# Kernel optimization log

Hardware: AMD Instinct MI355X
Metric: run time of the kernel (lower is better)

Reference implementation:

```python
import jax, jax.numpy as jnp
import numpy as np

OUT = 50000   # out_features = connectivity rows
IN = 50000    # in_features  = connectivity cols
NNZ = 1_600_000  # avg degree 32
B = 512       # batch (leading dims of x)


def setup_inputs() -> dict:
    key = jax.random.key(0)
    k1, k2, k3, k4 = jax.random.split(key, 4)
    x = jax.random.normal(k1, (B, IN), dtype=jnp.float32)
    rows = jax.random.randint(k2, (NNZ,), 0, OUT, dtype=jnp.int32)
    cols = jax.random.randint(k3, (NNZ,), 0, IN, dtype=jnp.int32)
    indices = jnp.stack([rows, cols])            # [2, NNZ] COO indices
    values = jax.random.normal(k4, (NNZ,), dtype=jnp.float32)
    bias = jnp.zeros((OUT, 1), dtype=jnp.float32)  # module initializes bias to zeros
    return {"x": x, "indices": indices, "values": values, "bias": bias}


def reference(x, indices, values, bias):
    # feature_dim=-1: permute features to dim 0 -> x_t is (IN, B)
    row, col = indices[0], indices[1]
    x_t = x.T                                    # (IN, B)
    # spmm: for each nnz, values[e] * x_t[col[e]] accumulated into row[e]
    contrib = values[:, None] * x_t[col]         # (NNZ, B)
    y = jax.ops.segment_sum(contrib, row, num_segments=OUT)  # (OUT, B)
    y = y + bias                                 # bias is (OUT, 1), broadcasts
    return y.T                                   # permute back -> (B, OUT)
```

## Files before the change

### kernel.cpp

```cpp
#include <hip/hip_runtime.h>
#include <hip/hip_bf16.h>


typedef float f32x4 __attribute__((ext_vector_type(4)));

#define CAP 96

__global__ void zero_i32_kernel(int* __restrict__ p, int n) {
    int i = blockIdx.x * blockDim.x + threadIdx.x;
    if (i < n) p[i] = 0;
}

__global__ __launch_bounds__(256) void build_kernel(
        const float* __restrict__ x, __hip_bfloat16* __restrict__ xT,
        int rows_x, int cols_x, int tbx, int tbtot,
        const int* __restrict__ erows, const int* __restrict__ ecols,
        const float* __restrict__ evals, int nnz,
        int* __restrict__ cursor, int2* __restrict__ edges) {
    __shared__ __hip_bfloat16 T[64][72];
    const int bid = blockIdx.x;

    if (bid < tbtot) {
        const int bx = bid % tbx;
        const int by = bid / tbx;
        const int c0 = bx * 64;
        const int r0 = by * 64;
        const int t  = threadIdx.x;

        {
            const int tx = t & 15, ty = t >> 4;
            const int c = c0 + tx * 4;
            for (int p = 0; p < 4; ++p) {
                const int rl = ty + p * 16;
                const int r = r0 + rl;
                float fx = 0.f, fy = 0.f, fz = 0.f, fw = 0.f;
                if (r < rows_x && c + 3 < cols_x) {
                    f32x4 f = __builtin_nontemporal_load(
                        (const f32x4*)(x + (size_t)r * cols_x + c));
                    fx = f.x; fy = f.y; fz = f.z; fw = f.w;
                } else if (r < rows_x) {
                    const float* p0 = x + (size_t)r * cols_x;
                    if (c + 0 < cols_x) fx = p0[c + 0];
                    if (c + 1 < cols_x) fy = p0[c + 1];
                    if (c + 2 < cols_x) fz = p0[c + 2];
                    if (c + 3 < cols_x) fw = p0[c + 3];
                }
                T[tx * 4 + 0][rl] = __float2bfloat16(fx);
                T[tx * 4 + 1][rl] = __float2bfloat16(fy);
                T[tx * 4 + 2][rl] = __float2bfloat16(fz);
                T[tx * 4 + 3][rl] = __float2bfloat16(fw);
            }
        }
        __syncthreads();
        {
            const int cl0 = t >> 3;
            const int rq  = t & 7;
            const int rl  = rq * 8;
            const int r   = r0 + rl;
            for (int q = 0; q < 2; ++q) {
                const int cl = q * 32 + cl0;
                const int c  = c0 + cl;
                if (c < cols_x) {
                    if (r + 7 < rows_x) {
                        *(uint4*)(xT + (size_t)c * rows_x + r) =
                            *(const uint4*)&T[cl][rl];
                    } else {
                        for (int j = 0; j < 8 && r + j < rows_x; ++j)
                            xT[(size_t)c * rows_x + r + j] = T[cl][rl + j];
                    }
                }
            }
        }
    } else {
        const int e = (bid - tbtot) * 256 + threadIdx.x;
        if (e < nnz) {
            const int   r = __builtin_nontemporal_load(erows + e);
            const int   c = __builtin_nontemporal_load(ecols + e);
            const float v = __builtin_nontemporal_load(evals + e);
            const int   p = atomicAdd(&cursor[r], 1);
            if (p < CAP)
                edges[(size_t)r * CAP + p] = make_int2(c, __float_as_int(v));
        }
    }
}

__device__ __forceinline__ float bf_lo(unsigned u) {
    return __uint_as_float(u << 16);
}
__device__ __forceinline__ float bf_hi(unsigned u) {
    return __uint_as_float(u & 0xffff0000u);
}

__device__ __forceinline__ void row_accum(
        const ushort* __restrict__ xb, const int2* __restrict__ edges,
        int e0, int e1, int B,
        float& a0, float& a1, float& a2, float& a3,
        float& a4, float& a5, float& a6, float& a7) {
    int e = e0;
    for (; e + 2 <= e1; e += 2) {
        const int2 d0 = edges[e];
        const int2 d1 = edges[e + 1];
        const uint4 u0 = *(const uint4*)(xb + (size_t)d0.x * B);
        const uint4 u1 = *(const uint4*)(xb + (size_t)d1.x * B);
        const float v0 = __int_as_float(d0.y);
        const float v1 = __int_as_float(d1.y);
        a0 += v0 * bf_lo(u0.x); a1 += v0 * bf_hi(u0.x);
        a2 += v0 * bf_lo(u0.y); a3 += v0 * bf_hi(u0.y);
        a4 += v0 * bf_lo(u0.z); a5 += v0 * bf_hi(u0.z);
        a6 += v0 * bf_lo(u0.w); a7 += v0 * bf_hi(u0.w);
        a0 += v1 * bf_lo(u1.x); a1 += v1 * bf_hi(u1.x);
        a2 += v1 * bf_lo(u1.y); a3 += v1 * bf_hi(u1.y);
        a4 += v1 * bf_lo(u1.z); a5 += v1 * bf_hi(u1.z);
        a6 += v1 * bf_lo(u1.w); a7 += v1 * bf_hi(u1.w);
    }
    if (e < e1) {
        const int2 d0 = edges[e];
        const uint4 u0 = *(const uint4*)(xb + (size_t)d0.x * B);
        const float v0 = __int_as_float(d0.y);
        a0 += v0 * bf_lo(u0.x); a1 += v0 * bf_hi(u0.x);
        a2 += v0 * bf_lo(u0.y); a3 += v0 * bf_hi(u0.y);
        a4 += v0 * bf_lo(u0.z); a5 += v0 * bf_hi(u0.z);
        a6 += v0 * bf_lo(u0.w); a7 += v0 * bf_hi(u0.w);
    }
}

__global__ __launch_bounds__(1024) void spmm_fused_kernel(
        const ushort* __restrict__ xT,
        const int* __restrict__ cursor,
        const int2* __restrict__ edges,
        const float* __restrict__ bias,
        float* __restrict__ outp,
        int OUTn) {
    __shared__ float Ty[16][516];
    const int w    = threadIdx.x >> 6;
    const int lane = threadIdx.x & 63;
    const int r    = blockIdx.x * 16 + w;
    const int B    = 512;

    float a0 = 0.f, a1 = 0.f, a2 = 0.f, a3 = 0.f;
    float a4 = 0.f, a5 = 0.f, a6 = 0.f, a7 = 0.f;
    {
        const int deg = min(cursor[r], CAP);
        const int e0  = r * CAP;
        const float bv = bias[r];
        const ushort* xb = xT + (size_t)(lane << 3);
        row_accum(xb, edges, e0, e0 + deg, B, a0, a1, a2, a3, a4, a5, a6, a7);
        a0 += bv; a1 += bv; a2 += bv; a3 += bv;
        a4 += bv; a5 += bv; a6 += bv; a7 += bv;
    }

    {
        float* p = &Ty[w][lane << 3];
        f32x4 f0, f1;
        f0.x = a0; f0.y = a1; f0.z = a2; f0.w = a3;
        f1.x = a4; f1.y = a5; f1.z = a6; f1.w = a7;
        *(f32x4*)(p)     = f0;
        *(f32x4*)(p + 4) = f1;
    }
    __syncthreads();
    {
        const int b  = threadIdx.x & 511;
        const int rq = (threadIdx.x >> 9) << 3;
        f32x4 f0, f1;
        f0.x = Ty[rq + 0][b]; f0.y = Ty[rq + 1][b];
        f0.z = Ty[rq + 2][b]; f0.w = Ty[rq + 3][b];
        f1.x = Ty[rq + 4][b]; f1.y = Ty[rq + 5][b];
        f1.z = Ty[rq + 6][b]; f1.w = Ty[rq + 7][b];
        float* op = outp + (size_t)b * OUTn + blockIdx.x * 16 + rq;
        *(f32x4*)(op)     = f0;
        *(f32x4*)(op + 4) = f1;
    }
}

__global__ __launch_bounds__(256) void spmm_kernel(
        const ushort* __restrict__ xT,
        const int* __restrict__ cursor,
        const int2* __restrict__ edges,
        const float* __restrict__ bias,
        float* __restrict__ y,
        int B, int OUTn) {
    const int lane = threadIdx.x & 63;
    const int r = blockIdx.x * 4 + (threadIdx.x >> 6);
    if (r >= OUTn) return;
    const int deg = min(cursor[r], CAP);
    const int e0  = r * CAP;
    const float bv = bias[r];
    const ushort* xb = xT + (size_t)(lane << 3);

    float a0 = 0.f, a1 = 0.f, a2 = 0.f, a3 = 0.f;
    float a4 = 0.f, a5 = 0.f, a6 = 0.f, a7 = 0.f;
    row_accum(xb, edges, e0, e0 + deg, B, a0, a1, a2, a3, a4, a5, a6, a7);

    float* yp = y + (size_t)r * B + (size_t)(lane << 3);
    *(float4*)(yp)     = make_float4(a0 + bv, a1 + bv, a2 + bv, a3 + bv);
    *(float4*)(yp + 4) = make_float4(a4 + bv, a5 + bv, a6 + bv, a7 + bv);
}

__global__ __launch_bounds__(256) void transpose32_v2(
        const float* __restrict__ in,
        float* __restrict__ out,
        int rows, int cols) {
    __shared__ float T[64][68];
    const int t  = threadIdx.x;
    const int c0 = blockIdx.x * 64;
    const int r0 = blockIdx.y * 64;
    {
        const int tx = t & 15, ty = t >> 4;
        const int c = c0 + tx * 4;
        for (int p = 0; p < 4; ++p) {
            const int rl = ty + p * 16;
            const int r = r0 + rl;
            float fx = 0.f, fy = 0.f, fz = 0.f, fw = 0.f;
            if (r < rows && c + 3 < cols) {
                const float4 f = *(const float4*)(in + (size_t)r * cols + c);
                fx = f.x; fy = f.y; fz = f.z; fw = f.w;
            } else if (r < rows) {
                const float* p0 = in + (size_t)r * cols;
                if (c + 0 < cols) fx = p0[c + 0];
                if (c + 1 < cols) fy = p0[c + 1];
                if (c + 2 < cols) fz = p0[c + 2];
                if (c + 3 < cols) fw = p0[c + 3];
            }
            T[tx * 4 + 0][rl] = fx;
            T[tx * 4 + 1][rl] = fy;
            T[tx * 4 + 2][rl] = fz;
            T[tx * 4 + 3][rl] = fw;
        }
    }
    __syncthreads();
    {
        const int rq  = t & 15;
        const int cl0 = t >> 4;
        const int rl  = rq * 4;
        const int r   = r0 + rl;
        for (int p = 0; p < 4; ++p) {
            const int cl = p * 16 + cl0;
            const int c  = c0 + cl;
            if (c < cols) {
                if (r + 3 < rows) {
                    f32x4 f;
                    f.x = T[cl][rl + 0]; f.y = T[cl][rl + 1];
                    f.z = T[cl][rl + 2]; f.w = T[cl][rl + 3];
                    __builtin_nontemporal_store(
                        f, (f32x4*)(out + (size_t)c * rows + r));
                } else {
                    for (int j = 0; j < 4 && r + j < rows; ++j)
                        out[(size_t)c * rows + r + j] = T[cl][rl + j];
                }
            }
        }
    }
}

extern "C" void kernel_launch(void* const* d_in, const int* in_sizes, int n_in,
                              void* d_out, int out_size, void* d_ws, size_t ws_size,
                              hipStream_t stream) {
    const float* x       = (const float*)d_in[0];
    const int*   indices = (const int*)  d_in[1];
    const float* values  = (const float*)d_in[2];
    const float* bias    = (const float*)d_in[3];

    float* out = (float*)d_out;

    const int NNZ = in_sizes[2];
    const int OUT = in_sizes[3];
    const int B   = out_size / OUT;
    const int IN  = (int)((size_t)in_sizes[0] / (size_t)B);
    (void)n_in; (void)ws_size;

    const int* rows = indices;
    const int* cols = indices + NNZ;

    char* ws = (char*)d_ws;
    __hip_bfloat16* xT = (__hip_bfloat16*)ws;  ws += (size_t)IN * B * sizeof(__hip_bfloat16);
    int2* edges  = (int2*)ws;  ws += (size_t)OUT * CAP * sizeof(int2);
    int*  cursor = (int*)ws;   ws += (size_t)OUT * sizeof(int);
    float* y     = (float*)ws;

    const int tbx   = (IN + 63) / 64;
    const int tby   = (B + 63) / 64;
    const int tbtot = tbx * tby;
    const int abks  = (NNZ + 255) / 256;

    zero_i32_kernel<<<(OUT + 255) / 256, 256, 0, stream>>>(cursor, OUT);

    build_kernel<<<tbtot + abks, 256, 0, stream>>>(
        x, xT, B, IN, tbx, tbtot, rows, cols, values, NNZ, cursor, edges);

    if (B == 512 && (OUT & 15) == 0) {
        spmm_fused_kernel<<<OUT / 16, 1024, 0, stream>>>(
            (const ushort*)xT, cursor, edges, bias, out, OUT);
    } else {
        spmm_kernel<<<(OUT + 3) / 4, 256, 0, stream>>>(
            (const ushort*)xT, cursor, edges, bias, y, B, OUT);
        transpose32_v2<<<dim3((B + 63) / 64, (OUT + 63) / 64), 256, 0, stream>>>(
            y, out, OUT, B);
    }
}
```

Before: 534.1 us.

## Bucket edges by column quarter and split batch across two blocks

Edges are now binned per output row into four column sub-ranges, so each row's gathers walk xT in column order. The fused SpMM kernel is split so each block handles half of the batch columns (256), with each lane loading 8 bytes instead of 16. This doubles the grid and is meant to improve locality and cache reuse of gathered xT rows. The cost is re-reading edge lists twice, more atomic slots, and a per-bucket cap of 48 that could drop edges if a row's degree is skewed.

```diff
diff --git a/kernel.cpp b/kernel.cpp
--- a/kernel.cpp
+++ b/kernel.cpp
@@ -4,7 +4,8 @@
 
 typedef float f32x4 __attribute__((ext_vector_type(4)));
 
-#define CAP 96
+#define NSUB 4
+#define CAPS 48
 
 __global__ void zero_i32_kernel(int* __restrict__ p, int n) {
     int i = blockIdx.x * blockDim.x + threadIdx.x;
@@ -15,7 +16,7 @@
         const float* __restrict__ x, __hip_bfloat16* __restrict__ xT,
         int rows_x, int cols_x, int tbx, int tbtot,
         const int* __restrict__ erows, const int* __restrict__ ecols,
-        const float* __restrict__ evals, int nnz,
+        const float* __restrict__ evals, int nnz, float inv_quart,
         int* __restrict__ cursor, int2* __restrict__ edges) {
     __shared__ __hip_bfloat16 T[64][72];
     const int bid = blockIdx.x;
@@ -77,9 +78,12 @@
             const int   r = __builtin_nontemporal_load(erows + e);
             const int   c = __builtin_nontemporal_load(ecols + e);
             const float v = __builtin_nontemporal_load(evals + e);
-            const int   p = atomicAdd(&cursor[r], 1);
-            if (p < CAP)
-                edges[(size_t)r * CAP + p] = make_int2(c, __float_as_int(v));
+            int sb = (int)((float)c * inv_quart);
+            sb = (sb > NSUB - 1) ? NSUB - 1 : sb;
+            const int k = r * NSUB + sb;
+            const int p = atomicAdd(&cursor[k], 1);
+            if (p < CAPS)
+                edges[(size_t)k * CAPS + p] = make_int2(c, __float_as_int(v));
         }
     }
 }
@@ -91,36 +95,29 @@
     return __uint_as_float(u & 0xffff0000u);
 }
 
-__device__ __forceinline__ void row_accum(
+__device__ __forceinline__ void row_accum4(
         const ushort* __restrict__ xb, const int2* __restrict__ edges,
-        int e0, int e1, int B,
-        float& a0, float& a1, float& a2, float& a3,
-        float& a4, float& a5, float& a6, float& a7) {
+        int e0, int e1,
+        float& a0, float& a1, float& a2, float& a3) {
     int e = e0;
     for (; e + 2 <= e1; e += 2) {
         const int2 d0 = edges[e];
         const int2 d1 = edges[e + 1];
-        const uint4 u0 = *(const uint4*)(xb + (size_t)d0.x * B);
-        const uint4 u1 = *(const uint4*)(xb + (size_t)d1.x * B);
+        const uint2 u0 = *(const uint2*)(xb + (size_t)d0.x * 512);
+        const uint2 u1 = *(const uint2*)(xb + (size_t)d1.x * 512);
         const float v0 = __int_as_float(d0.y);
         const float v1 = __int_as_float(d1.y);
         a0 += v0 * bf_lo(u0.x); a1 += v0 * bf_hi(u0.x);
         a2 += v0 * bf_lo(u0.y); a3 += v0 * bf_hi(u0.y);
-        a4 += v0 * bf_lo(u0.z); a5 += v0 * bf_hi(u0.z);
-        a6 += v0 * bf_lo(u0.w); a7 += v0 * bf_hi(u0.w);
         a0 += v1 * bf_lo(u1.x); a1 += v1 * bf_hi(u1.x);
         a2 += v1 * bf_lo(u1.y); a3 += v1 * bf_hi(u1.y);
-        a4 += v1 * bf_lo(u1.z); a5 += v1 * bf_hi(u1.z);
-        a6 += v1 * bf_lo(u1.w); a7 += v1 * bf_hi(u1.w);
     }
     if (e < e1) {
         const int2 d0 = edges[e];
-        const uint4 u0 = *(const uint4*)(xb + (size_t)d0.x * B);
+        const uint2 u0 = *(const uint2*)(xb + (size_t)d0.x * 512);
         const float v0 = __int_as_float(d0.y);
         a0 += v0 * bf_lo(u0.x); a1 += v0 * bf_hi(u0.x);
         a2 += v0 * bf_lo(u0.y); a3 += v0 * bf_hi(u0.y);
-        a4 += v0 * bf_lo(u0.z); a5 += v0 * bf_hi(u0.z);
-        a6 += v0 * bf_lo(u0.w); a7 += v0 * bf_hi(u0.w);
     }
 }
 
@@ -131,44 +128,44 @@
         const float* __restrict__ bias,
         float* __restrict__ outp,
         int OUTn) {
-    __shared__ float Ty[16][516];
+    __shared__ float Ty[16][260];
+    const int nrb  = OUTn >> 4;
+    const int half = (blockIdx.x >= nrb) ? 1 : 0;
+    const int rb   = blockIdx.x - half * nrb;
     const int w    = threadIdx.x >> 6;
     const int lane = threadIdx.x & 63;
-    const int r    = blockIdx.x * 16 + w;
-    const int B    = 512;
+    const int r    = rb * 16 + w;
 
     float a0 = 0.f, a1 = 0.f, a2 = 0.f, a3 = 0.f;
-    float a4 = 0.f, a5 = 0.f, a6 = 0.f, a7 = 0.f;
-    {
-        const int deg = min(cursor[r], CAP);
-        const int e0  = r * CAP;
+    {
         const float bv = bias[r];
-        const ushort* xb = xT + (size_t)(lane << 3);
-        row_accum(xb, edges, e0, e0 + deg, B, a0, a1, a2, a3, a4, a5, a6, a7);
+        const ushort* xb = xT + half * 256 + (lane << 2);
+        const int4 c4 = *(const int4*)(cursor + r * NSUB);
+        int base = r * NSUB * CAPS;
+        row_accum4(xb, edges, base, base + min(c4.x, CAPS), a0, a1, a2, a3);
+        base += CAPS;
+        row_accum4(xb, edges, base, base + min(c4.y, CAPS), a0, a1, a2, a3);
+        base += CAPS;
+        row_accum4(xb, edges, base, base + min(c4.z, CAPS), a0, a1, a2, a3);
+        base += CAPS;
+        row_accum4(xb, edges, base, base + min(c4.w, CAPS), a0, a1, a2, a3);
         a0 += bv; a1 += bv; a2 += bv; a3 += bv;
-        a4 += bv; a5 += bv; a6 += bv; a7 += bv;
-    }
-
-    {
-        float* p = &Ty[w][lane << 3];
-        f32x4 f0, f1;
-        f0.x = a0; f0.y = a1; f0.z = a2; f0.w = a3;
-        f1.x = a4; f1.y = a5; f1.z = a6; f1.w = a7;
-        *(f32x4*)(p)     = f0;
-        *(f32x4*)(p + 4) = f1;
+    }
+
+    {
+        f32x4 f;
+        f.x = a0; f.y = a1; f.z = a2; f.w = a3;
+        *(f32x4*)&Ty[w][lane << 2] = f;
     }
     __syncthreads();
     {
-        const int b  = threadIdx.x & 511;
-        const int rq = (threadIdx.x >> 9) << 3;
-        f32x4 f0, f1;
-        f0.x = Ty[rq + 0][b]; f0.y = Ty[rq + 1][b];
-        f0.z = Ty[rq + 2][b]; f0.w = Ty[rq + 3][b];
-        f1.x = Ty[rq + 4][b]; f1.y = Ty[rq + 5][b];
-        f1.z = Ty[rq + 6][b]; f1.w = Ty[rq + 7][b];
-        float* op = outp + (size_t)b * OUTn + blockIdx.x * 16 + rq;
-        *(f32x4*)(op)     = f0;
-        *(f32x4*)(op + 4) = f1;
+        const int b    = threadIdx.x >> 2;
+        const int rsel = (threadIdx.x & 3) << 2;
+        f32x4 f;
+        f.x = Ty[rsel + 0][b]; f.y = Ty[rsel + 1][b];
+        f.z = Ty[rsel + 2][b]; f.w = Ty[rsel + 3][b];
+        float* op = outp + (size_t)(half * 256 + b) * OUTn + rb * 16 + rsel;
+        *(f32x4*)op = f;
     }
 }
 
@@ -182,14 +179,25 @@
     const int lane = threadIdx.x & 63;
     const int r = blockIdx.x * 4 + (threadIdx.x >> 6);
     if (r >= OUTn) return;
-    const int deg = min(cursor[r], CAP);
-    const int e0  = r * CAP;
     const float bv = bias[r];
     const ushort* xb = xT + (size_t)(lane << 3);
 
     float a0 = 0.f, a1 = 0.f, a2 = 0.f, a3 = 0.f;
     float a4 = 0.f, a5 = 0.f, a6 = 0.f, a7 = 0.f;
-    row_accum(xb, edges, e0, e0 + deg, B, a0, a1, a2, a3, a4, a5, a6, a7);
+    for (int sb = 0; sb < NSUB; ++sb) {
+        const int k  = r * NSUB + sb;
+        const int e0 = k * CAPS;
+        const int e1 = e0 + min(cursor[k], CAPS);
+        for (int e = e0; e < e1; ++e) {
+            const int2 d0 = edges[e];
+            const uint4 u0 = *(const uint4*)(xb + (size_t)d0.x * B);
+            const float v0 = __int_as_float(d0.y);
+            a0 += v0 * bf_lo(u0.x); a1 += v0 * bf_hi(u0.x);
+            a2 += v0 * bf_lo(u0.y); a3 += v0 * bf_hi(u0.y);
+            a4 += v0 * bf_lo(u0.z); a5 += v0 * bf_hi(u0.z);
+            a6 += v0 * bf_lo(u0.w); a7 += v0 * bf_hi(u0.w);
+        }
+    }
 
     float* yp = y + (size_t)r * B + (size_t)(lane << 3);
     *(float4*)(yp)     = make_float4(a0 + bv, a1 + bv, a2 + bv, a3 + bv);
@@ -273,22 +281,25 @@
 
     char* ws = (char*)d_ws;
     __hip_bfloat16* xT = (__hip_bfloat16*)ws;  ws += (size_t)IN * B * sizeof(__hip_bfloat16);
-    int2* edges  = (int2*)ws;  ws += (size_t)OUT * CAP * sizeof(int2);
-    int*  cursor = (int*)ws;   ws += (size_t)OUT * sizeof(int);
+    int2* edges  = (int2*)ws;  ws += (size_t)OUT * NSUB * CAPS * sizeof(int2);
+    int*  cursor = (int*)ws;   ws += (size_t)OUT * NSUB * sizeof(int);
     float* y     = (float*)ws;
 
     const int tbx   = (IN + 63) / 64;
     const int tby   = (B + 63) / 64;
     const int tbtot = tbx * tby;
     const int abks  = (NNZ + 255) / 256;
-
-    zero_i32_kernel<<<(OUT + 255) / 256, 256, 0, stream>>>(cursor, OUT);
+    const float inv_quart = (float)NSUB / (float)IN;
+
+    zero_i32_kernel<<<(OUT * NSUB + 255) / 256, 256, 0, stream>>>(
+        cursor, OUT * NSUB);
 
     build_kernel<<<tbtot + abks, 256, 0, stream>>>(
-        x, xT, B, IN, tbx, tbtot, rows, cols, values, NNZ, cursor, edges);
+        x, xT, B, IN, tbx, tbtot, rows, cols, values, NNZ, inv_quart,
+        cursor, edges);
 
     if (B == 512 && (OUT & 15) == 0) {
-        spmm_fused_kernel<<<OUT / 16, 1024, 0, stream>>>(
+        spmm_fused_kernel<<<2 * (OUT / 16), 1024, 0, stream>>>(
             (const ushort*)xT, cursor, edges, bias, out, OUT);
     } else {
         spmm_kernel<<<(OUT + 3) / 4, 256, 0, stream>>>(
```

After: 553.9 us. 3.7% more time.
